# Kernel optimization log

Hardware: AMD Instinct MI355X
Metric: run time of the kernel (lower is better)

Reference implementation:

```python
import jax, jax.numpy as jnp
import numpy as np

EPS = 1e-12  # torch spectral_norm default eps


def _l2norm(v):
    return v / (jnp.linalg.norm(v) + EPS)


def _spectral_norm_2d(w, u):
    # one power iteration (torch default n_power_iterations=1), u/v detached
    v = _l2norm(w.T @ u)
    u_new = _l2norm(w @ v)
    u_new = jax.lax.stop_gradient(u_new)
    v = jax.lax.stop_gradient(v)
    sigma = u_new @ (w @ v)
    return w / sigma


def _spectral_norm_1d(b):
    # torch._SpectralNorm for ndim==1: F.normalize(weight, dim=0)
    return b / (jnp.linalg.norm(b) + EPS)


def setup_inputs() -> dict:
    key = jax.random.key(0)
    ks = jax.random.split(key, 8)
    T, B, I, H = 4096, 32, 256, 256
    s_i = 1.0 / np.sqrt(H)  # nn.RNN init: U(-1/sqrt(H), 1/sqrt(H))
    return {
        "x": jax.random.normal(ks[0], (T, B, I), jnp.float32),
        "state": jax.random.normal(ks[1], (1, B, H), jnp.float32),
        "w_ih": jax.random.uniform(ks[2], (H, I), jnp.float32, -s_i, s_i),
        "w_hh": jax.random.uniform(ks[3], (H, H), jnp.float32, -s_i, s_i),
        "b_ih": jax.random.uniform(ks[4], (H,), jnp.float32, -s_i, s_i),
        "b_hh": jax.random.uniform(ks[5], (H,), jnp.float32, -s_i, s_i),
        "u_ih": jax.random.normal(ks[6], (H,), jnp.float32),  # power-iteration buffer
        "u_hh": jax.random.normal(ks[7], (H,), jnp.float32),
    }


def reference(x, state, w_ih, w_hh, b_ih, b_hh, u_ih, u_hh):
    # spectral-norm parametrization of all RNN weights
    w_ih_sn = _spectral_norm_2d(w_ih, _l2norm(u_ih))
    w_hh_sn = _spectral_norm_2d(w_hh, _l2norm(u_hh))
    b_sn = _spectral_norm_1d(b_ih) + _spectral_norm_1d(b_hh)

    # input projection batched over all timesteps: [T,B,H]
    pre = jnp.einsum("tbi,hi->tbh", x, w_ih_sn) + b_sn

    def step(h, p):
        h_new = jnp.tanh(p + h @ w_hh_sn.T)
        return h_new, h_new

    h_last, out = jax.lax.scan(step, state[0], pre)
    return out, h_last[None]
```

## Files before the change

### kernel.cpp

```cpp
#include <hip/hip_runtime.h>
#include <hip/hip_bf16.h>
#include <math.h>

#define EPSF 1e-12f
#define H 256
#define TSTEPS 4096
#define BATCH 32
#define TB (TSTEPS*BATCH)
#define BH (BATCH*H)

typedef _Float16 h2 __attribute__((ext_vector_type(2)));

#define BC(u) __builtin_bit_cast(h2, (u))

#define DPPF(x, ctrl) __builtin_bit_cast(float, __builtin_amdgcn_update_dpp( \
    0, __builtin_bit_cast(int, (x)), (ctrl), 0xf, 0xf, true))
#define DPP_QUAD_XOR1 0xB1
#define DPP_QUAD_XOR2 0x4E
#define DPP_HALF_MIRROR 0x141
#define DPP_ROW_MIRROR  0x140

__device__ __forceinline__ void bar_nodrain() {
  __builtin_amdgcn_sched_barrier(0);
  asm volatile("s_waitcnt lgkmcnt(0)" ::: "memory");
  __builtin_amdgcn_s_barrier();
  __builtin_amdgcn_sched_barrier(0);
}

__device__ __forceinline__ float block_sum256(float v, float* red) {
  #pragma unroll
  for (int o = 32; o > 0; o >>= 1) v += __shfl_down(v, o, 64);
  __syncthreads();
  if ((threadIdx.x & 63) == 0) red[threadIdx.x >> 6] = v;
  __syncthreads();
  return red[0] + red[1] + red[2] + red[3];
}

__global__ __launch_bounds__(256) void k_prep(
    const float* __restrict__ w_ih, const float* __restrict__ w_hh,
    const float* __restrict__ b_ih, const float* __restrict__ b_hh,
    const float* __restrict__ u_ih, const float* __restrict__ u_hh,
    float* __restrict__ wsc) {
  __shared__ float red[4];
  __shared__ float ubuf[H];
  __shared__ float vbuf[H];
  const int tid = threadIdx.x;

  float inv_sig[2];
  const float* Ws[2] = {w_ih, w_hh};
  const float* Us[2] = {u_ih, u_hh};
  #pragma unroll 1
  for (int m = 0; m < 2; m++) {
    const float* W = Ws[m];
    float uv = Us[m][tid];
    float nu = sqrtf(block_sum256(uv * uv, red));
    ubuf[tid] = uv / (nu + EPSF);
    __syncthreads();
    float vt = 0.f;
    for (int h = 0; h < H; h++) vt = fmaf(W[h * H + tid], ubuf[h], vt);
    float nv = sqrtf(block_sum256(vt * vt, red));
    vbuf[tid] = vt / (nv + EPSF);
    __syncthreads();
    float wv = 0.f;
    const float* wr = W + (size_t)tid * H;
    for (int i = 0; i < H; i++) wv = fmaf(wr[i], vbuf[i], wv);
    float n2 = block_sum256(wv * wv, red);
    float sigma = n2 / (sqrtf(n2) + EPSF);
    inv_sig[m] = 1.f / sigma;
  }
  float bi = b_ih[tid], bh = b_hh[tid];
  float nbi = sqrtf(block_sum256(bi * bi, red));
  float nbh = sqrtf(block_sum256(bh * bh, red));
  wsc[tid] = bi / (nbi + EPSF) + bh / (nbh + EPSF);
  if (tid == 0) { wsc[H] = inv_sig[0]; wsc[H + 1] = inv_sig[1]; }
}

__global__ __launch_bounds__(256) void k_wcvt(
    const float* __restrict__ w_ih, const float* __restrict__ wsc,
    _Float16* __restrict__ wt) {
  const int h = blockIdx.x, k = threadIdx.x;
  wt[(size_t)k * H + h] = (_Float16)(w_ih[(size_t)h * H + k] * wsc[H]);
}

__global__ __launch_bounds__(256) void k_pre(
    const float* __restrict__ x, const _Float16* __restrict__ wt,
    const float* __restrict__ wsc, float* __restrict__ pre) {
  __shared__ float xs[64 * 256];
  const int tid = threadIdx.x;
  const size_t m0 = (size_t)blockIdx.x * 64;

  const float4* xp = (const float4*)(x + m0 * H);
  float4* xsv = (float4*)xs;
  #pragma unroll
  for (int j = 0; j < 16; j++) xsv[j * 256 + tid] = xp[j * 256 + tid];
  __syncthreads();

  const int hg = tid & 31;
  const int mg = tid >> 5;
  const int h0 = hg << 3;
  const int mr0 = mg << 3;

  float acc[8][8];
  #pragma unroll
  for (int i = 0; i < 8; i++)
    #pragma unroll
    for (int j = 0; j < 8; j++) acc[i][j] = 0.f;

  #pragma unroll 1
  for (int kb = 0; kb < 256; kb += 4) {
    float wf[4][8];
    #pragma unroll
    for (int j = 0; j < 4; j++) {
      uint4 wv = *(const uint4*)(wt + (size_t)(kb + j) * H + h0);
      h2 p0 = BC(wv.x), p1 = BC(wv.y), p2 = BC(wv.z), p3 = BC(wv.w);
      wf[j][0] = (float)p0.x; wf[j][1] = (float)p0.y;
      wf[j][2] = (float)p1.x; wf[j][3] = (float)p1.y;
      wf[j][4] = (float)p2.x; wf[j][5] = (float)p2.y;
      wf[j][6] = (float)p3.x; wf[j][7] = (float)p3.y;
    }
    #pragma unroll
    for (int i = 0; i < 8; i++) {
      float4 xv = *(const float4*)(xs + (mr0 + i) * 256 + kb);
      #pragma unroll
      for (int j = 0; j < 8; j++) {
        float a = acc[i][j];
        a = fmaf(xv.x, wf[0][j], a);
        a = fmaf(xv.y, wf[1][j], a);
        a = fmaf(xv.z, wf[2][j], a);
        a = fmaf(xv.w, wf[3][j], a);
        acc[i][j] = a;
      }
    }
  }
  float bs[8];
  #pragma unroll
  for (int j = 0; j < 8; j++) bs[j] = wsc[h0 + j];
  #pragma unroll
  for (int i = 0; i < 8; i++) {
    float4 o0, o1;
    o0.x = acc[i][0] + bs[0];
    o0.y = acc[i][1] + bs[1];
    o0.z = acc[i][2] + bs[2];
    o0.w = acc[i][3] + bs[3];
    o1.x = acc[i][4] + bs[4];
    o1.y = acc[i][5] + bs[5];
    o1.z = acc[i][6] + bs[6];
    o1.w = acc[i][7] + bs[7];
    float* pr = pre + (m0 + mr0 + i) * H + h0;
    *(float4*)pr = o0;
    *(float4*)(pr + 4) = o1;
  }
}

__global__ __launch_bounds__(512, 1) void k_scan(
    const float* __restrict__ state, const float* __restrict__ w_hh,
    const float* __restrict__ wsc, float* __restrict__ out) {
  __shared__ __align__(16) float hbuf[2][320];
  const int tid = threadIdx.x;
  const int cg   = tid >> 6;
  const int q    = tid & 63;
  const int rgrp = q >> 4;
  const int kseg = q & 15;
  const int jrow = 4 * ((q >> 3) & 1) + 2 * ((q >> 2) & 1) + ((q >> 1) & 1);
  const int myrow = (cg << 5) + (rgrp << 3) + jrow;
  const int b = blockIdx.x;
  const float inv_s = wsc[H + 1];
  const bool hb3 = (q >> 3) & 1, hb2 = (q >> 2) & 1, hb1 = (q >> 1) & 1;

  float wreg[8][16];
  #pragma unroll
  for (int i = 0; i < 8; i++) {
    const float* wr = w_hh + (size_t)((cg << 5) + (rgrp << 3) + i) * H + (kseg << 4);
    #pragma unroll
    for (int c4 = 0; c4 < 4; c4++) {
      float4 wv = *(const float4*)(wr + (c4 << 2));
      wreg[i][c4 * 4 + 0] = wv.x * inv_s;
      wreg[i][c4 * 4 + 1] = wv.y * inv_s;
      wreg[i][c4 * 4 + 2] = wv.z * inv_s;
      wreg[i][c4 * 4 + 3] = wv.w * inv_s;
    }
  }

  const int rbase = kseg * 20;
  const int wpub  = myrow + ((myrow >> 4) << 2);

  if (tid < H) hbuf[0][tid + ((tid >> 4) << 2)] = state[b * H + tid];

  const float* pbase = out + (size_t)b * H + myrow;
  float pre0 = pbase[0], pre1 = pbase[BH];
  bar_nodrain();

  float hn = 0.f;
  #pragma unroll 1
  for (int t = 0; t < TSTEPS; t++) {
    int tn = (t + 2 <= TSTEPS) ? (t + 2) : TSTEPS;
    float pre2 = pbase[(size_t)tn * BH];

    const float* hb = hbuf[t & 1];
    float4 r0 = *(const float4*)(hb + rbase);
    float4 r1 = *(const float4*)(hb + rbase + 4);
    float4 r2 = *(const float4*)(hb + rbase + 8);
    float4 r3 = *(const float4*)(hb + rbase + 12);
    float hk[16] = {r0.x, r0.y, r0.z, r0.w, r1.x, r1.y, r1.z, r1.w,
                    r2.x, r2.y, r2.z, r2.w, r3.x, r3.y, r3.z, r3.w};

    float acc[8];
    #pragma unroll
    for (int i = 0; i < 8; i++) {
      float a = 0.f;
      #pragma unroll
      for (int c = 0; c < 16; c++) a = fmaf(wreg[i][c], hk[c], a);
      acc[i] = a;
    }

    float v0, v1, v2, v3;
    { float k0 = hb3 ? acc[4] : acc[0], s0 = hb3 ? acc[0] : acc[4];
      float k1 = hb3 ? acc[5] : acc[1], s1 = hb3 ? acc[1] : acc[5];
      float k2 = hb3 ? acc[6] : acc[2], s2 = hb3 ? acc[2] : acc[6];
      float k3 = hb3 ? acc[7] : acc[3], s3 = hb3 ? acc[3] : acc[7];
      v0 = k0 + DPPF(s0, DPP_ROW_MIRROR);
      v1 = k1 + DPPF(s1, DPP_ROW_MIRROR);
      v2 = k2 + DPPF(s2, DPP_ROW_MIRROR);
      v3 = k3 + DPPF(s3, DPP_ROW_MIRROR); }
    float u0, u1;
    { float k0 = hb2 ? v2 : v0, s0 = hb2 ? v0 : v2;
      float k1 = hb2 ? v3 : v1, s1 = hb2 ? v1 : v3;
      u0 = k0 + DPPF(s0, DPP_HALF_MIRROR);
      u1 = k1 + DPPF(s1, DPP_HALF_MIRROR); }
    float ssum;
    { float k0 = hb1 ? u1 : u0, s0 = hb1 ? u0 : u1;
      ssum = k0 + DPPF(s0, DPP_QUAD_XOR2); }
    ssum += DPPF(ssum, DPP_QUAD_XOR1);

    float s = ssum + pre0;
    float sc = fminf(fmaxf(s, -15.f), 15.f);
    float e = __expf(2.f * sc);
    hn = __fdividef(e - 1.f, e + 1.f);

    if (!(q & 1)) {
      hbuf[(t + 1) & 1][wpub] = hn;
      out[(size_t)t * BH + b * H + myrow] = hn;
    }
    bar_nodrain();
    pre0 = pre1; pre1 = pre2;
  }
  if (!(q & 1)) out[(size_t)TSTEPS * BH + b * H + myrow] = hn;
}

extern "C" void kernel_launch(void* const* d_in, const int* in_sizes, int n_in,
                              void* d_out, int out_size, void* d_ws, size_t ws_size,
                              hipStream_t stream) {
  const float* x     = (const float*)d_in[0];
  const float* state = (const float*)d_in[1];
  const float* w_ih  = (const float*)d_in[2];
  const float* w_hh  = (const float*)d_in[3];
  const float* b_ih  = (const float*)d_in[4];
  const float* b_hh  = (const float*)d_in[5];
  const float* u_ih  = (const float*)d_in[6];
  const float* u_hh  = (const float*)d_in[7];
  float* out = (float*)d_out;
  float* wsc = (float*)d_ws;
  _Float16* wt = (_Float16*)((char*)d_ws + 2048);

  k_prep<<<1, 256, 0, stream>>>(w_ih, w_hh, b_ih, b_hh, u_ih, u_hh, wsc);
  k_wcvt<<<H, 256, 0, stream>>>(w_ih, wsc, wt);
  k_pre<<<TB / 64, 256, 0, stream>>>(x, wt, wsc, out);
  k_scan<<<BATCH, 512, 0, stream>>>(state, w_hh, wsc, out);
}
```

Baseline: 2.721 ms.

## Double scan block to 1024 threads, halving rows per thread

The recurrent scan kernel now launches 1024 threads per batch block instead of 512, and each thread holds 4 weight rows instead of 8. The per-step FMA chain and the DPP reduction tree get shorter, which is meant to cut the latency of each serial timestep. In exchange the block needs more waves per barrier, so each step's sync covers 16 wavefronts, and a quarter of the lanes now publish results.

```diff
diff --git a/kernel.cpp b/kernel.cpp
--- a/kernel.cpp
+++ b/kernel.cpp
@@ -152,25 +152,25 @@
   }
 }
 
-__global__ __launch_bounds__(512, 1) void k_scan(
+__global__ __launch_bounds__(1024, 1) void k_scan(
     const float* __restrict__ state, const float* __restrict__ w_hh,
     const float* __restrict__ wsc, float* __restrict__ out) {
   __shared__ __align__(16) float hbuf[2][320];
   const int tid = threadIdx.x;
-  const int cg   = tid >> 6;
+  const int w    = tid >> 6;
   const int q    = tid & 63;
-  const int rgrp = q >> 4;
+  const int rgrp = (q >> 4) & 3;
   const int kseg = q & 15;
-  const int jrow = 4 * ((q >> 3) & 1) + 2 * ((q >> 2) & 1) + ((q >> 1) & 1);
-  const int myrow = (cg << 5) + (rgrp << 3) + jrow;
+  const bool hb3 = (q >> 3) & 1, hb2 = (q >> 2) & 1;
+  const int r0 = (w << 4) + (rgrp << 2);
+  const int myrow = r0 + 2 * (int)hb3 + (int)hb2;
   const int b = blockIdx.x;
   const float inv_s = wsc[H + 1];
-  const bool hb3 = (q >> 3) & 1, hb2 = (q >> 2) & 1, hb1 = (q >> 1) & 1;
-
-  float wreg[8][16];
-  #pragma unroll
-  for (int i = 0; i < 8; i++) {
-    const float* wr = w_hh + (size_t)((cg << 5) + (rgrp << 3) + i) * H + (kseg << 4);
+
+  float wreg[4][16];
+  #pragma unroll
+  for (int i = 0; i < 4; i++) {
+    const float* wr = w_hh + (size_t)(r0 + i) * H + (kseg << 4);
     #pragma unroll
     for (int c4 = 0; c4 < 4; c4++) {
       float4 wv = *(const float4*)(wr + (c4 << 2));
@@ -197,39 +197,31 @@
     float pre2 = pbase[(size_t)tn * BH];
 
     const float* hb = hbuf[t & 1];
-    float4 r0 = *(const float4*)(hb + rbase);
-    float4 r1 = *(const float4*)(hb + rbase + 4);
-    float4 r2 = *(const float4*)(hb + rbase + 8);
-    float4 r3 = *(const float4*)(hb + rbase + 12);
-    float hk[16] = {r0.x, r0.y, r0.z, r0.w, r1.x, r1.y, r1.z, r1.w,
-                    r2.x, r2.y, r2.z, r2.w, r3.x, r3.y, r3.z, r3.w};
-
-    float acc[8];
-    #pragma unroll
-    for (int i = 0; i < 8; i++) {
+    float4 rv0 = *(const float4*)(hb + rbase);
+    float4 rv1 = *(const float4*)(hb + rbase + 4);
+    float4 rv2 = *(const float4*)(hb + rbase + 8);
+    float4 rv3 = *(const float4*)(hb + rbase + 12);
+    float hk[16] = {rv0.x, rv0.y, rv0.z, rv0.w, rv1.x, rv1.y, rv1.z, rv1.w,
+                    rv2.x, rv2.y, rv2.z, rv2.w, rv3.x, rv3.y, rv3.z, rv3.w};
+
+    float acc[4];
+    #pragma unroll
+    for (int i = 0; i < 4; i++) {
       float a = 0.f;
       #pragma unroll
       for (int c = 0; c < 16; c++) a = fmaf(wreg[i][c], hk[c], a);
       acc[i] = a;
     }
 
-    float v0, v1, v2, v3;
-    { float k0 = hb3 ? acc[4] : acc[0], s0 = hb3 ? acc[0] : acc[4];
-      float k1 = hb3 ? acc[5] : acc[1], s1 = hb3 ? acc[1] : acc[5];
-      float k2 = hb3 ? acc[6] : acc[2], s2 = hb3 ? acc[2] : acc[6];
-      float k3 = hb3 ? acc[7] : acc[3], s3 = hb3 ? acc[3] : acc[7];
+    float v0, v1;
+    { float k0 = hb3 ? acc[2] : acc[0], s0 = hb3 ? acc[0] : acc[2];
+      float k1 = hb3 ? acc[3] : acc[1], s1 = hb3 ? acc[1] : acc[3];
       v0 = k0 + DPPF(s0, DPP_ROW_MIRROR);
-      v1 = k1 + DPPF(s1, DPP_ROW_MIRROR);
-      v2 = k2 + DPPF(s2, DPP_ROW_MIRROR);
-      v3 = k3 + DPPF(s3, DPP_ROW_MIRROR); }
-    float u0, u1;
-    { float k0 = hb2 ? v2 : v0, s0 = hb2 ? v0 : v2;
-      float k1 = hb2 ? v3 : v1, s1 = hb2 ? v1 : v3;
-      u0 = k0 + DPPF(s0, DPP_HALF_MIRROR);
-      u1 = k1 + DPPF(s1, DPP_HALF_MIRROR); }
+      v1 = k1 + DPPF(s1, DPP_ROW_MIRROR); }
     float ssum;
-    { float k0 = hb1 ? u1 : u0, s0 = hb1 ? u0 : u1;
-      ssum = k0 + DPPF(s0, DPP_QUAD_XOR2); }
+    { float k0 = hb2 ? v1 : v0, s0 = hb2 ? v0 : v1;
+      ssum = k0 + DPPF(s0, DPP_HALF_MIRROR); }
+    ssum += DPPF(ssum, DPP_QUAD_XOR2);
     ssum += DPPF(ssum, DPP_QUAD_XOR1);
 
     float s = ssum + pre0;
@@ -237,14 +229,14 @@
     float e = __expf(2.f * sc);
     hn = __fdividef(e - 1.f, e + 1.f);
 
-    if (!(q & 1)) {
+    if ((q & 3) == 0) {
       hbuf[(t + 1) & 1][wpub] = hn;
       out[(size_t)t * BH + b * H + myrow] = hn;
     }
     bar_nodrain();
     pre0 = pre1; pre1 = pre2;
   }
-  if (!(q & 1)) out[(size_t)TSTEPS * BH + b * H + myrow] = hn;
+  if ((q & 3) == 0) out[(size_t)TSTEPS * BH + b * H + myrow] = hn;
 }
 
 extern "C" void kernel_launch(void* const* d_in, const int* in_sizes, int n_in,
@@ -265,5 +257,5 @@
   k_prep<<<1, 256, 0, stream>>>(w_ih, w_hh, b_ih, b_hh, u_ih, u_hh, wsc);
   k_wcvt<<<H, 256, 0, stream>>>(w_ih, wsc, wt);
   k_pre<<<TB / 64, 256, 0, stream>>>(x, wt, wsc, out);
-  k_scan<<<BATCH, 512, 0, stream>>>(state, w_hh, wsc, out);
-}
+  k_scan<<<BATCH, 1024, 0, stream>>>(state, w_hh, wsc, out);
+}
```

After: 2.809 ms. +3.2%, slower.
